# Performance work log

Hardware: AMD Instinct MI355X
Metric: run time of the kernel (lower is better)

Reference implementation:

```python
import jax, jax.numpy as jnp
import numpy as np
import math

D_MODEL = 1024
NUM_HEADS = 16
D_K = D_MODEL // NUM_HEADS
MAX_SEQ_LEN = 2048
THETA = 10000.0
BATCH = 2
SEQ = 2048


def setup_inputs() -> dict:
    key = jax.random.key(0)
    ks = jax.random.split(key, 5)
    std = math.sqrt(2.0 / (D_MODEL + D_MODEL))
    def w(k):
        return jnp.clip(std * jax.random.normal(k, (D_MODEL, D_MODEL), dtype=jnp.float32), -3 * std, 3 * std)
    return {
        "x": jax.random.normal(ks[0], (BATCH, SEQ, D_MODEL), dtype=jnp.float32),
        "token_positions": jnp.arange(SEQ, dtype=jnp.int32),
        "Wq": w(ks[1]),
        "Wk": w(ks[2]),
        "Wv": w(ks[3]),
        "Wo": w(ks[4]),
    }


def _rope_tables():
    inv_freq = 1.0 / THETA ** (jnp.arange(0, D_K, 2, dtype=jnp.float32) / D_K)  # [d_k/2]
    positions = jnp.arange(MAX_SEQ_LEN, dtype=jnp.float32)[:, None]             # [max_seq, 1]
    angles = positions * inv_freq                                               # [max_seq, d_k/2]
    return jnp.cos(angles), jnp.sin(angles)


def _apply_rope(x, cos, sin):
    # x: [..., seq, d_k]; cos/sin: [seq, d_k/2] (broadcast over leading dims)
    x1, x2 = x[..., ::2], x[..., 1::2]
    r1 = x1 * cos - x2 * sin
    r2 = x1 * sin + x2 * cos
    return jnp.stack((r1, r2), axis=-1).reshape(x.shape)


def reference(x, token_positions, Wq, Wk, Wv, Wo):
    B, S, D = x.shape
    def proj(W):
        y = jnp.einsum('bsd,od->bso', x, W)
        return y.reshape(B, S, NUM_HEADS, D_K).transpose(0, 2, 1, 3)  # [B,H,S,dk]
    q, k, v = proj(Wq), proj(Wk), proj(Wv)

    cos_t, sin_t = _rope_tables()
    cos, sin = cos_t[token_positions], sin_t[token_positions]  # [S, d_k/2]
    q = _apply_rope(q, cos, sin)
    k = _apply_rope(k, cos, sin)

    scores = jnp.einsum('bhqd,bhkd->bhqk', q, k) / math.sqrt(D_K)
    causal = jnp.tril(jnp.ones((S, S), dtype=bool))
    scores = jnp.where(causal, scores, -jnp.inf)
    attn = jax.nn.softmax(scores, axis=-1)
    out = jnp.einsum('bhqk,bhkd->bhqd', attn, v)
    out = out.transpose(0, 2, 1, 3).reshape(B, S, D)
    return jnp.einsum('bsd,od->bso', out, Wo)
```

## Files before the change

### kernel.cpp

```cpp
#include <hip/hip_runtime.h>
#include <hip/hip_bf16.h>


typedef __attribute__((ext_vector_type(8))) short short8;
typedef __attribute__((ext_vector_type(4))) float floatx4;

static __device__ __forceinline__ unsigned short f2bf(float f) {
  __hip_bfloat16 h = __float2bfloat16(f);
  return *(unsigned short*)&h;
}

static __device__ __forceinline__ unsigned int pk2bf(float a, float b) {
  unsigned int ua = __float_as_uint(a) + 0x8000u;
  unsigned int ub = __float_as_uint(b) + 0x8000u;
  return __builtin_amdgcn_perm(ub, ua, 0x07060302u);
}

static __device__ __forceinline__ float fexp2(float x) {
  float r;
  asm("v_exp_f32 %0, %1\n\ts_nop 0" : "=v"(r) : "v"(x));
  return r;
}

static __device__ __forceinline__ void gl2lds16(const unsigned short* g,
                                                unsigned short* l) {
  __builtin_amdgcn_global_load_lds(
      (const __attribute__((address_space(1))) void*)g,
      (__attribute__((address_space(3))) void*)l, 16, 0, 0);
}

__global__ __launch_bounds__(256) void cvt_all(
    const float4* __restrict__ x,  const float4* __restrict__ wq,
    const float4* __restrict__ wk, const float4* __restrict__ wv,
    const float4* __restrict__ wo,
    ushort4* __restrict__ xb,  ushort4* __restrict__ wqb,
    ushort4* __restrict__ wkb, ushort4* __restrict__ wvb,
    ushort4* __restrict__ wob,
    const int* __restrict__ tokpos,
    float* __restrict__ ctab, float* __restrict__ stab) {
  int t = blockIdx.y;
  int i = blockIdx.x * 256 + threadIdx.x;
  if (t == 5) {
    if (i < 65536) {
      int s = i >> 5, f = i & 31;
      float inv = expf(-9.210340371976184f * (float)(2 * f) / 64.0f);
      float ang = (float)tokpos[s] * inv;
      ctab[i] = cosf(ang);
      stab[i] = sinf(ang);
    }
    return;
  }
  const float4* s = (t == 0) ? x : (t == 1) ? wq : (t == 2) ? wk : (t == 3) ? wv : wo;
  ushort4* d = (t == 0) ? xb : (t == 1) ? wqb : (t == 2) ? wkb : (t == 3) ? wvb : wob;
  int n4 = (t == 0) ? 1048576 : 262144;
  if (i < n4) {
    float4 v = s[i];
    ushort4 o;
    o.x = f2bf(v.x); o.y = f2bf(v.y); o.z = f2bf(v.z); o.w = f2bf(v.w);
    d[i] = o;
  }
}

#define GEMM128_BODY(Aptr, Wptr, m0, n0)                                        \
  __shared__ __align__(16) unsigned short lA[128 * 64];                         \
  __shared__ __align__(16) unsigned short lB[128 * 64];                         \
  int tid = threadIdx.x;                                                        \
  int wave = tid >> 6, lane = tid & 63;                                         \
  int wm = wave >> 1, wn = wave & 1;                                            \
  int l15 = lane & 15, quad = lane >> 4;                                        \
  int srow = wave * 32 + (lane >> 3);                   \
  int sch = lane & 7;                                   \
  int fsw = l15 & 7;                                 \
  floatx4 acc[4][4];                                                            \
  _Pragma("unroll") for (int m = 0; m < 4; ++m)                                 \
      _Pragma("unroll") for (int n = 0; n < 4; ++n)                             \
          acc[m][n] = (floatx4){0.f, 0.f, 0.f, 0.f};                            \
  for (int kt = 0; kt < 16; ++kt) {                                             \
    _Pragma("unroll") for (int p = 0; p < 4; ++p) {                             \
      int r = srow + p * 8;                                                     \
      int g = sch ^ (r & 7);                                                    \
      gl2lds16(Aptr + (size_t)(m0 + r) * 1024 + kt * 64 + g * 8,                \
               lA + (wave * 32 + p * 8) * 64);                                  \
      gl2lds16(Wptr + (size_t)(n0 + r) * 1024 + kt * 64 + g * 8,                \
               lB + (wave * 32 + p * 8) * 64);                                  \
    }                                                                           \
    __syncthreads();                                                            \
    _Pragma("unroll") for (int ks = 0; ks < 2; ++ks) {                          \
      short8 af[4], bf[4];                                                      \
      _Pragma("unroll") for (int m = 0; m < 4; ++m)                             \
          af[m] = *(const short8*)(lA + (wm * 64 + m * 16 + l15) * 64 +         \
                                   (((ks * 4 + quad) ^ fsw) * 8));              \
      _Pragma("unroll") for (int n = 0; n < 4; ++n)                             \
          bf[n] = *(const short8*)(lB + (wn * 64 + n * 16 + l15) * 64 +         \
                                   (((ks * 4 + quad) ^ fsw) * 8));              \
      _Pragma("unroll") for (int m = 0; m < 4; ++m)                             \
          _Pragma("unroll") for (int n = 0; n < 4; ++n)                         \
              acc[m][n] = __builtin_amdgcn_mfma_f32_16x16x32_bf16(              \
                  af[m], bf[n], acc[m][n], 0, 0, 0);                            \
    }                                                                           \
    __syncthreads();                                                            \
  }

__global__ __launch_bounds__(256) void qkv_mfma(
    const unsigned short* __restrict__ X,
    const unsigned short* __restrict__ Wq,
    const unsigned short* __restrict__ Wk,
    const unsigned short* __restrict__ Wv,
    const float* __restrict__ ctab, const float* __restrict__ stab,
    unsigned short* __restrict__ Qo, unsigned short* __restrict__ Ko,
    unsigned short* __restrict__ Vo) {
  int mat = blockIdx.z;
  const unsigned short* W = (mat == 0) ? Wq : ((mat == 1) ? Wk : Wv);
  unsigned short* Out = (mat == 0) ? Qo : ((mat == 1) ? Ko : Vo);
  int m0 = blockIdx.x * 128, n0 = blockIdx.y * 128;

  GEMM128_BODY(X, W, m0, n0)

#pragma unroll
  for (int n = 0; n < 4; ++n) {
    int col = n0 + wn * 64 + n * 16 + l15;
    int h = col >> 6;
    int d = col & 63;
    int pi = d >> 1;
    bool odd = (d & 1) != 0;
    size_t hb = (size_t)h * 2048 * 64;
#pragma unroll
    for (int m = 0; m < 4; ++m) {
      int row0 = m0 + wm * 64 + m * 16 + quad * 4;
      int b = row0 >> 11;
      int s0 = row0 & 2047;
      size_t base = (size_t)b * 16 * 2048 * 64 + hb;
      if (mat == 2) {
        ushort4 pv;
        pv.x = f2bf(acc[m][n][0]);
        pv.y = f2bf(acc[m][n][1]);
        pv.z = f2bf(acc[m][n][2]);
        pv.w = f2bf(acc[m][n][3]);
        *(ushort4*)(Out + base + (size_t)d * 2048 + s0) = pv;
      } else {
#pragma unroll
        for (int i = 0; i < 4; ++i) {
          int s = s0 + i;
          float v = acc[m][n][i];
          float p = __shfl_xor(v, 1);
          float c = ctab[s * 32 + pi];
          float sn = stab[s * 32 + pi];
          float res = odd ? fmaf(p, sn, v * c) : fmaf(v, c, -p * sn);
          if (mat == 0) res *= 0.1803368801111204f;
          Out[base + (size_t)s * 64 + d] = f2bf(res);
        }
      }
    }
  }
}

__global__ __launch_bounds__(256) void oproj_mfma(
    const unsigned short* __restrict__ A, const unsigned short* __restrict__ Wo,
    float* __restrict__ Out) {
  __shared__ __align__(16) unsigned short lA[64 * 64];
  __shared__ __align__(16) unsigned short lB[128 * 64];
  int tid = threadIdx.x;
  int wave = tid >> 6, lane = tid & 63;
  int l15 = lane & 15, quad = lane >> 4;
  int rsub = lane >> 3, sch = lane & 7;
  int fsw = l15 & 7;
  int m0 = blockIdx.x * 64, n0 = blockIdx.y * 128;

  floatx4 acc[4][2];
#pragma unroll
  for (int m = 0; m < 4; ++m)
#pragma unroll
    for (int n = 0; n < 2; ++n) acc[m][n] = (floatx4){0.f, 0.f, 0.f, 0.f};

  for (int kt = 0; kt < 16; ++kt) {
#pragma unroll
    for (int p = 0; p < 2; ++p) {
      int r = wave * 16 + p * 8 + rsub;
      int g = sch ^ (r & 7);
      gl2lds16(A + (size_t)(m0 + r) * 1024 + kt * 64 + g * 8,
               lA + (wave * 16 + p * 8) * 64);
    }
#pragma unroll
    for (int p = 0; p < 4; ++p) {
      int r = wave * 32 + p * 8 + rsub;
      int g = sch ^ (r & 7);
      gl2lds16(Wo + (size_t)(n0 + r) * 1024 + kt * 64 + g * 8,
               lB + (wave * 32 + p * 8) * 64);
    }
    __syncthreads();
#pragma unroll
    for (int ks = 0; ks < 2; ++ks) {
      int slot = ((ks * 4 + quad) ^ fsw) * 8;
      short8 af[4], bf[2];
#pragma unroll
      for (int m = 0; m < 4; ++m)
        af[m] = *(const short8*)(lA + (m * 16 + l15) * 64 + slot);
#pragma unroll
      for (int n = 0; n < 2; ++n)
        bf[n] = *(const short8*)(lB + (wave * 32 + n * 16 + l15) * 64 + slot);
#pragma unroll
      for (int m = 0; m < 4; ++m)
#pragma unroll
        for (int n = 0; n < 2; ++n)
          acc[m][n] = __builtin_amdgcn_mfma_f32_16x16x32_bf16(
              af[m], bf[n], acc[m][n], 0, 0, 0);
    }
    __syncthreads();
  }

#pragma unroll
  for (int m = 0; m < 4; ++m) {
#pragma unroll
    for (int n = 0; n < 2; ++n) {
      int col = n0 + wave * 32 + n * 16 + l15;
#pragma unroll
      for (int i = 0; i < 4; ++i) {
        int row = m0 + m * 16 + quad * 4 + i;
        Out[(size_t)row * 1024 + col] = acc[m][n][i];
      }
    }
  }
}

#define LPS 72

__global__ __launch_bounds__(256) void attn_flash(
    const unsigned short* __restrict__ Q, const unsigned short* __restrict__ K,
    const unsigned short* __restrict__ Vt, unsigned short* __restrict__ Oc) {
  __shared__ __align__(16) unsigned short lK[64 * 64];
  __shared__ __align__(16) unsigned short lV[64 * 64];
  __shared__ unsigned short lP[4][16 * LPS];

  int tid = threadIdx.x;
  int wave = tid >> 6, lane = tid & 63;
  int l15 = lane & 15, quad = lane >> 4;

  int xb_ = blockIdx.x;
  int yb_ = blockIdx.y;
  int jb = yb_ >> 3, ib = yb_ & 7;
  int qtile;
  if (jb == 0)      qtile = xb_;
  else if (jb == 1) qtile = 31 - xb_;
  else if (jb == 2) qtile = (15 - xb_) & 31;
  else              qtile = (16 + xb_) & 31;
  int bh = ib * 4 + jb;

  size_t base = (size_t)bh * 2048 * 64;
  int qbase = qtile * 64;

  const unsigned short* qrow = Q + base + (size_t)(qbase + wave * 16 + l15) * 64;
  short8 qb0 = *(const short8*)(qrow + quad * 8);
  short8 qb1 = *(const short8*)(qrow + 32 + quad * 8);

  floatx4 o[4];
  float m_i = -1e30f, l_i = 0.f;
#pragma unroll
  for (int n = 0; n < 4; ++n) o[n] = (floatx4){0.f, 0.f, 0.f, 0.f};

  int r0 = tid >> 3, g = tid & 7;
  int r1 = r0 + 32;
  int e0 = g * 8;
  int sl = (g ^ (r0 & 7)) * 8;
  int fsw = l15 & 7;
  int c0 = (quad ^ fsw) * 8;
  int c1 = ((quad + 4) ^ fsw) * 8;

  const unsigned short* kp = K + base;
  const unsigned short* vp = Vt + base;
  short8 pk0 = *(const short8*)(kp + r0 * 64 + e0);
  short8 pk1 = *(const short8*)(kp + r1 * 64 + e0);
  short8 pv0 = *(const short8*)(vp + (size_t)r0 * 2048 + e0);
  short8 pv1 = *(const short8*)(vp + (size_t)r1 * 2048 + e0);

  for (int kt = 0; kt <= qtile; ++kt) {
    __syncthreads();
    *(short8*)(lK + r0 * 64 + sl) = pk0;
    *(short8*)(lK + r1 * 64 + sl) = pk1;
    *(short8*)(lV + r0 * 64 + sl) = pv0;
    *(short8*)(lV + r1 * 64 + sl) = pv1;
    __syncthreads();

    if (kt < qtile) {
      const unsigned short* kn = K + base + (size_t)(kt + 1) * 4096;
      const unsigned short* vn = Vt + base + (kt + 1) * 64;
      pk0 = *(const short8*)(kn + r0 * 64 + e0);
      pk1 = *(const short8*)(kn + r1 * 64 + e0);
      pv0 = *(const short8*)(vn + (size_t)r0 * 2048 + e0);
      pv1 = *(const short8*)(vn + (size_t)r1 * 2048 + e0);
    }

    float sc[4][4];
#pragma unroll
    for (int sub = 0; sub < 4; ++sub) {
      const unsigned short* kr = lK + (sub * 16 + l15) * 64;
      short8 a0 = *(const short8*)(kr + c0);
      short8 a1 = *(const short8*)(kr + c1);
      floatx4 s = {0.f, 0.f, 0.f, 0.f};
      s = __builtin_amdgcn_mfma_f32_16x16x32_bf16(a0, qb0, s, 0, 0, 0);
      s = __builtin_amdgcn_mfma_f32_16x16x32_bf16(a1, qb1, s, 0, 0, 0);
#pragma unroll
      for (int i = 0; i < 4; ++i) sc[sub][i] = s[i];
    }

    if (kt == qtile) {
      int qin = wave * 16 + l15;
#pragma unroll
      for (int sub = 0; sub < 4; ++sub)
#pragma unroll
        for (int i = 0; i < 4; ++i)
          if (sub * 16 + quad * 4 + i > qin) sc[sub][i] = -1e30f;
    }

    float mb = sc[0][0];
#pragma unroll
    for (int sub = 0; sub < 4; ++sub)
#pragma unroll
      for (int i = 0; i < 4; ++i) mb = fmaxf(mb, sc[sub][i]);
    mb = fmaxf(mb, __shfl_xor(mb, 16));
    mb = fmaxf(mb, __shfl_xor(mb, 32));

    float mn = fmaxf(m_i, mb);
    float al = fexp2(m_i - mn);
    m_i = mn;
    float rs = 0.f;
#pragma unroll
    for (int sub = 0; sub < 4; ++sub)
#pragma unroll
      for (int i = 0; i < 4; ++i) {
        float p = fexp2(sc[sub][i] - mn);
        sc[sub][i] = p;
        rs += p;
      }
    rs += __shfl_xor(rs, 16);
    rs += __shfl_xor(rs, 32);
    l_i = l_i * al + rs;

#pragma unroll
    for (int n = 0; n < 4; ++n) {
      o[n][0] *= al; o[n][1] *= al; o[n][2] *= al; o[n][3] *= al;
    }

    unsigned short* pw = lP[wave] + l15 * LPS;
#pragma unroll
    for (int sub = 0; sub < 4; ++sub) {
      uint2 w;
      w.x = pk2bf(sc[sub][0], sc[sub][1]);
      w.y = pk2bf(sc[sub][2], sc[sub][3]);
      *(uint2*)(pw + sub * 16 + quad * 4) = w;
    }

    const unsigned short* pr = lP[wave] + l15 * LPS + quad * 8;
    short8 pa0 = *(const short8*)(pr);
    short8 pa1 = *(const short8*)(pr + 32);

#pragma unroll
    for (int n = 0; n < 4; ++n) {
      const unsigned short* vr = lV + (n * 16 + l15) * 64;
      short8 vb0 = *(const short8*)(vr + c0);
      short8 vb1 = *(const short8*)(vr + c1);
      o[n] = __builtin_amdgcn_mfma_f32_16x16x32_bf16(vb0, pa0, o[n], 0, 0, 0);
      o[n] = __builtin_amdgcn_mfma_f32_16x16x32_bf16(vb1, pa1, o[n], 0, 0, 0);
    }
  }

  int b = bh >> 4, h = bh & 15;
  float inv = 1.f / l_i;
  int s = qbase + wave * 16 + l15;
  size_t orow = (size_t)(b * 2048 + s) * 1024 + h * 64;
#pragma unroll
  for (int n = 0; n < 4; ++n) {
    uint2 ov;
    ov.x = pk2bf(o[n][0] * inv, o[n][1] * inv);
    ov.y = pk2bf(o[n][2] * inv, o[n][3] * inv);
    *(uint2*)(Oc + orow + n * 16 + quad * 4) = ov;
  }
}

extern "C" void kernel_launch(void* const* d_in, const int* in_sizes, int n_in,
                              void* d_out, int out_size, void* d_ws, size_t ws_size,
                              hipStream_t stream) {
  const float* x  = (const float*)d_in[0];
  const int* tokpos = (const int*)d_in[1];
  const float* Wq = (const float*)d_in[2];
  const float* Wk = (const float*)d_in[3];
  const float* Wv = (const float*)d_in[4];
  const float* Wo = (const float*)d_in[5];
  float* out = (float*)d_out;

  float* ws = (float*)d_ws;
  float* ctab = ws;
  float* stab = ctab + 65536;
  unsigned short* u = (unsigned short*)(stab + 65536);
  unsigned short* Qb  = u;
  unsigned short* Kb  = Qb + 4194304;
  unsigned short* Vb  = Kb + 4194304;
  unsigned short* Oc  = Vb + 4194304;
  unsigned short* xb  = Oc + 4194304;
  unsigned short* Wqb = xb + 4194304;
  unsigned short* Wkb = Wqb + 1048576;
  unsigned short* Wvb = Wkb + 1048576;
  unsigned short* Wob = Wvb + 1048576;

  cvt_all<<<dim3(4096, 6), 256, 0, stream>>>(
      (const float4*)x, (const float4*)Wq, (const float4*)Wk,
      (const float4*)Wv, (const float4*)Wo,
      (ushort4*)xb, (ushort4*)Wqb, (ushort4*)Wkb, (ushort4*)Wvb, (ushort4*)Wob,
      tokpos, ctab, stab);

  qkv_mfma<<<dim3(32, 8, 3), 256, 0, stream>>>(
      xb, Wqb, Wkb, Wvb, ctab, stab, Qb, Kb, Vb);
  attn_flash<<<dim3(32, 32), 256, 0, stream>>>(Qb, Kb, Vb, Oc);
  oproj_mfma<<<dim3(64, 8), 256, 0, stream>>>(Oc, Wob, out);
}
```

Before: 190.4 us.

## Double-buffer LDS tiles in QKV and output-projection GEMMs

Both projection GEMMs now use two LDS buffers per operand. The first K-tile is loaded before the loop, and each iteration issues the global-to-LDS copy for the next tile before running MFMAs on the current one. The barrier that used to sit between the load and the compute is dropped, so memory latency can overlap with matrix math. The cost is twice the LDS footprint (64 KB per block in the QKV GEMM), which may lower occupancy. Correctness also depends on the remaining end-of-iteration barrier waiting for the async LDS loads.

```diff
diff --git a/kernel.cpp b/kernel.cpp
--- a/kernel.cpp
+++ b/kernel.cpp
@@ -62,8 +62,8 @@
 }
 
 #define GEMM128_BODY(Aptr, Wptr, m0, n0)                                        \
-  __shared__ __align__(16) unsigned short lA[128 * 64];                         \
-  __shared__ __align__(16) unsigned short lB[128 * 64];                         \
+  __shared__ __align__(16) unsigned short lA[2][128 * 64];                      \
+  __shared__ __align__(16) unsigned short lB[2][128 * 64];                      \
   int tid = threadIdx.x;                                                        \
   int wave = tid >> 6, lane = tid & 63;                                         \
   int wm = wave >> 1, wn = wave & 1;                                            \
@@ -75,23 +75,34 @@
   _Pragma("unroll") for (int m = 0; m < 4; ++m)                                 \
       _Pragma("unroll") for (int n = 0; n < 4; ++n)                             \
           acc[m][n] = (floatx4){0.f, 0.f, 0.f, 0.f};                            \
+  _Pragma("unroll") for (int p = 0; p < 4; ++p) {                               \
+    int r = srow + p * 8;                                                       \
+    int g = sch ^ (r & 7);                                                      \
+    gl2lds16(Aptr + (size_t)(m0 + r) * 1024 + g * 8,                            \
+             lA[0] + (wave * 32 + p * 8) * 64);                                 \
+    gl2lds16(Wptr + (size_t)(n0 + r) * 1024 + g * 8,                            \
+             lB[0] + (wave * 32 + p * 8) * 64);                                 \
+  }                                                                             \
+  __syncthreads();                                                              \
   for (int kt = 0; kt < 16; ++kt) {                                             \
-    _Pragma("unroll") for (int p = 0; p < 4; ++p) {                             \
-      int r = srow + p * 8;                                                     \
-      int g = sch ^ (r & 7);                                                    \
-      gl2lds16(Aptr + (size_t)(m0 + r) * 1024 + kt * 64 + g * 8,                \
-               lA + (wave * 32 + p * 8) * 64);                                  \
-      gl2lds16(Wptr + (size_t)(n0 + r) * 1024 + kt * 64 + g * 8,                \
-               lB + (wave * 32 + p * 8) * 64);                                  \
+    int cur = kt & 1;                                                           \
+    if (kt < 15) {   \
+      _Pragma("unroll") for (int p = 0; p < 4; ++p) {                           \
+        int r = srow + p * 8;                                                   \
+        int g = sch ^ (r & 7);                                                  \
+        gl2lds16(Aptr + (size_t)(m0 + r) * 1024 + (kt + 1) * 64 + g * 8,        \
+                 lA[cur ^ 1] + (wave * 32 + p * 8) * 64);                       \
+        gl2lds16(Wptr + (size_t)(n0 + r) * 1024 + (kt + 1) * 64 + g * 8,        \
+                 lB[cur ^ 1] + (wave * 32 + p * 8) * 64);                       \
+      }                                                                         \
     }                                                                           \
-    __syncthreads();                                                            \
     _Pragma("unroll") for (int ks = 0; ks < 2; ++ks) {                          \
       short8 af[4], bf[4];                                                      \
       _Pragma("unroll") for (int m = 0; m < 4; ++m)                             \
-          af[m] = *(const short8*)(lA + (wm * 64 + m * 16 + l15) * 64 +         \
+          af[m] = *(const short8*)(lA[cur] + (wm * 64 + m * 16 + l15) * 64 +    \
                                    (((ks * 4 + quad) ^ fsw) * 8));              \
       _Pragma("unroll") for (int n = 0; n < 4; ++n)                             \
-          bf[n] = *(const short8*)(lB + (wn * 64 + n * 16 + l15) * 64 +         \
+          bf[n] = *(const short8*)(lB[cur] + (wn * 64 + n * 16 + l15) * 64 +    \
                                    (((ks * 4 + quad) ^ fsw) * 8));              \
       _Pragma("unroll") for (int m = 0; m < 4; ++m)                             \
           _Pragma("unroll") for (int n = 0; n < 4; ++n)                         \
@@ -157,8 +168,8 @@
 __global__ __launch_bounds__(256) void oproj_mfma(
     const unsigned short* __restrict__ A, const unsigned short* __restrict__ Wo,
     float* __restrict__ Out) {
-  __shared__ __align__(16) unsigned short lA[64 * 64];
-  __shared__ __align__(16) unsigned short lB[128 * 64];
+  __shared__ __align__(16) unsigned short lA[2][64 * 64];
+  __shared__ __align__(16) unsigned short lB[2][128 * 64];
   int tid = threadIdx.x;
   int wave = tid >> 6, lane = tid & 63;
   int l15 = lane & 15, quad = lane >> 4;
@@ -172,32 +183,48 @@
 #pragma unroll
     for (int n = 0; n < 2; ++n) acc[m][n] = (floatx4){0.f, 0.f, 0.f, 0.f};
 
+#pragma unroll
+  for (int p = 0; p < 2; ++p) {
+    int r = wave * 16 + p * 8 + rsub;
+    int g = sch ^ (r & 7);
+    gl2lds16(A + (size_t)(m0 + r) * 1024 + g * 8, lA[0] + (wave * 16 + p * 8) * 64);
+  }
+#pragma unroll
+  for (int p = 0; p < 4; ++p) {
+    int r = wave * 32 + p * 8 + rsub;
+    int g = sch ^ (r & 7);
+    gl2lds16(Wo + (size_t)(n0 + r) * 1024 + g * 8, lB[0] + (wave * 32 + p * 8) * 64);
+  }
+  __syncthreads();
+
   for (int kt = 0; kt < 16; ++kt) {
-#pragma unroll
-    for (int p = 0; p < 2; ++p) {
-      int r = wave * 16 + p * 8 + rsub;
-      int g = sch ^ (r & 7);
-      gl2lds16(A + (size_t)(m0 + r) * 1024 + kt * 64 + g * 8,
-               lA + (wave * 16 + p * 8) * 64);
-    }
-#pragma unroll
-    for (int p = 0; p < 4; ++p) {
-      int r = wave * 32 + p * 8 + rsub;
-      int g = sch ^ (r & 7);
-      gl2lds16(Wo + (size_t)(n0 + r) * 1024 + kt * 64 + g * 8,
-               lB + (wave * 32 + p * 8) * 64);
-    }
-    __syncthreads();
+    int cur = kt & 1;
+    if (kt < 15) {
+#pragma unroll
+      for (int p = 0; p < 2; ++p) {
+        int r = wave * 16 + p * 8 + rsub;
+        int g = sch ^ (r & 7);
+        gl2lds16(A + (size_t)(m0 + r) * 1024 + (kt + 1) * 64 + g * 8,
+                 lA[cur ^ 1] + (wave * 16 + p * 8) * 64);
+      }
+#pragma unroll
+      for (int p = 0; p < 4; ++p) {
+        int r = wave * 32 + p * 8 + rsub;
+        int g = sch ^ (r & 7);
+        gl2lds16(Wo + (size_t)(n0 + r) * 1024 + (kt + 1) * 64 + g * 8,
+                 lB[cur ^ 1] + (wave * 32 + p * 8) * 64);
+      }
+    }
 #pragma unroll
     for (int ks = 0; ks < 2; ++ks) {
       int slot = ((ks * 4 + quad) ^ fsw) * 8;
       short8 af[4], bf[2];
 #pragma unroll
       for (int m = 0; m < 4; ++m)
-        af[m] = *(const short8*)(lA + (m * 16 + l15) * 64 + slot);
+        af[m] = *(const short8*)(lA[cur] + (m * 16 + l15) * 64 + slot);
 #pragma unroll
       for (int n = 0; n < 2; ++n)
-        bf[n] = *(const short8*)(lB + (wave * 32 + n * 16 + l15) * 64 + slot);
+        bf[n] = *(const short8*)(lB[cur] + (wave * 32 + n * 16 + l15) * 64 + slot);
 #pragma unroll
       for (int m = 0; m < 4; ++m)
 #pragma unroll
```

Result: slower. 195.0 us (+2.4%).
